# Kernel tuning notes

Hardware: AMD Instinct MI355X
Metric: run time of the kernel (lower is better)

## Reference

```python
import jax, jax.numpy as jnp
import numpy as np

H = 32          # num attention heads
KVH = 8         # num key/value heads
D = 128         # head dim
THETA = 10000.0


def _rope_tables(kv_len):
    inv_freq = 1.0 / (THETA ** (jnp.arange(0, D, 2, dtype=jnp.float32) / D))  # [D/2]
    t = jnp.arange(kv_len, dtype=jnp.float32)
    freqs = jnp.outer(t, inv_freq)                  # [kv_len, D/2]
    emb = jnp.concatenate([freqs, freqs], axis=-1)  # [kv_len, D]
    return jnp.cos(emb), jnp.sin(emb)


def _rotate_half(x):
    x1, x2 = jnp.split(x, 2, axis=-1)
    return jnp.concatenate([-x2, x1], axis=-1)


def setup_inputs() -> dict:
    key = jax.random.key(0)
    ks = jax.random.split(key, 7)
    B, QL, KVL, HID = 4, 128, 4096, 4096
    hidden_states = jax.random.normal(ks[0], (B, QL, HID), jnp.float32)
    key_states = jax.random.normal(ks[1], (B, KVH, KVL, D), jnp.float32)
    value_states = jax.random.normal(ks[2], (B, KVH, KVL, D), jnp.float32)
    Wq = jax.random.normal(ks[3], (HID, H * D), jnp.float32) * (HID ** -0.5)
    Wo = jax.random.normal(ks[4], (H * D, HID), jnp.float32) * ((H * D) ** -0.5)
    position_ids = jnp.sort(jax.random.randint(ks[5], (B, KVL), 0, KVL), axis=-1).astype(jnp.int64)
    attention_mask = jax.random.randint(ks[6], (B, 1, QL, KVL), 0, 2) == 1
    return {"hidden_states": hidden_states, "key_states": key_states,
            "value_states": value_states, "Wq": Wq, "Wo": Wo,
            "position_ids": position_ids, "attention_mask": attention_mask}


def reference(hidden_states, key_states, value_states, Wq, Wo, position_ids, attention_mask):
    B, QL, HID = hidden_states.shape
    KVL = position_ids.shape[-1]

    # q projection -> [B, H, QL, D]
    q = (hidden_states @ Wq).reshape(B, QL, H, D).transpose(0, 2, 1, 3)

    # RoPE: apply rotation for the single max position per batch to all q positions
    cos, sin = _rope_tables(KVL)                               # [KVL, D]
    pos = jnp.take_along_axis(position_ids,
                              jnp.argmax(position_ids.astype(jnp.int32), axis=1)[:, None],
                              axis=1)                          # [B, 1]
    cos_b = cos[pos][:, None]                                  # [B, 1, 1, D]
    sin_b = sin[pos][:, None]
    q = q * cos_b + _rotate_half(q) * sin_b

    # GQA repeat kv heads -> [B, H, KVL, D]
    groups = H // KVH
    k = jnp.repeat(key_states, groups, axis=1)
    v = jnp.repeat(value_states, groups, axis=1)

    scores = jnp.einsum('bhqd,bhkd->bhqk', q, k) / jnp.sqrt(jnp.float32(D))
    scores = jnp.where(attention_mask, jnp.float32(-10000.0), scores)
    attn = jax.nn.softmax(scores.astype(jnp.float32), axis=-1).astype(q.dtype)

    out = jnp.einsum('bhqk,bhkd->bhqd', attn, v)               # [B, H, QL, D]
    out = out.transpose(0, 2, 1, 3).reshape(B, QL, H * D)
    return out @ Wo
```

## Files before the change

### kernel.cpp

```cpp
#include <hip/hip_runtime.h>
#include <math.h>

typedef __attribute__((ext_vector_type(8))) short bf16x8;
typedef __attribute__((ext_vector_type(4))) float f32x4;
typedef __attribute__((ext_vector_type(4))) short s16x4;
typedef __attribute__((ext_vector_type(4))) int i32x4;

__device__ inline unsigned short f2bf(float x){
  unsigned u = __builtin_bit_cast(unsigned, x);
  u = (u + 0x7FFFu + ((u >> 16) & 1u)) >> 16;
  return (unsigned short)u;
}
__device__ inline float bf2f(unsigned short v){
  return __builtin_bit_cast(float, (unsigned)v << 16);
}
__device__ inline unsigned pk2bf(float lo, float hi){
  return (unsigned)f2bf(lo) | ((unsigned)f2bf(hi) << 16);
}

__device__ inline void gl16(const void* g, void* l){
  __builtin_amdgcn_global_load_lds(
      (const __attribute__((address_space(1))) unsigned int*)g,
      (__attribute__((address_space(3))) unsigned int*)l, 16, 0, 0);
}

#define KVLEN 4096
#define QLEN  128
#define NH    32
#define NKVH  8
#define HD    128
#define HIDD  4096
#define NSPLIT 4
#define KVCHUNK (KVLEN / NSPLIT)

#define WSWZ(n) ((((unsigned)(n) & 7u) ^ (((unsigned)(n) >> 3) & 7u)) << 4)
#define VSWZ(byte) ((byte) ^ ((((byte) >> 11) & 7u) << 4))

__global__ void prep_kernel(const int* __restrict__ pos32,
                            float* __restrict__ costab,
                            float* __restrict__ sintab){
  int tid = threadIdx.x;
  int b = tid >> 6, j = tid & 63;
  bool pos64 = (pos32[2*4095 + 1] == 0);
  long long mpos;
  if (pos64) mpos = ((const long long*)pos32)[(size_t)b*KVLEN + KVLEN - 1];
  else       mpos = (long long)pos32[(size_t)b*KVLEN + KVLEN - 1];
  double inv = pow(10000.0, -((double)j) / 64.0);
  double ang = (double)mpos * inv;
  costab[b*64 + j] = (float)cos(ang);
  sintab[b*64 + j] = (float)sin(ang);
}

__global__ __launch_bounds__(256) void prepall_kernel(
    const float* __restrict__ Kg, const float* __restrict__ Vg,
    const float* __restrict__ Wq, const float* __restrict__ Wo,
    const float* __restrict__ hidden, const void* __restrict__ mask,
    const float* __restrict__ costab, const float* __restrict__ sintab,
    unsigned short* __restrict__ Kswz, unsigned short* __restrict__ V2,
    unsigned short* __restrict__ WqImg, unsigned short* __restrict__ WoImg,
    unsigned short* __restrict__ A1img,
    unsigned long long* __restrict__ bits){
  __shared__ alignas(16) char tl[16384];
  int bid = blockIdx.x, tid = threadIdx.x;

  if (bid < 2048){
    const unsigned int* m32 = (const unsigned int*)mask;
    unsigned long long det = __ballot((m32[tid & 63] & 0xFFFFFF00u) != 0);
    bool m8 = (det != 0);
#pragma unroll
    for (int it = 0; it < 4; ++it){
      int idx = bid * 1024 + it * 256 + tid;
      bool v = m8 ? (((const unsigned char*)mask)[idx] != 0)
                  : (((const int*)mask)[idx] != 0);
      unsigned long long bal = __ballot(v);
      if ((tid & 63) == 0) bits[idx >> 6] = bal;
    }

  } else if (bid < 4096){
    int t = bid - 2048;
    int b = t >> 9;
    const float* kin = Kg + (size_t)t * 8192;
    const float* vin = Vg + (size_t)t * 8192;
    unsigned short* kout = Kswz + (size_t)t * 8192;
    unsigned short* vout = V2   + (size_t)t * 8192;
#pragma unroll
    for (int i = 0; i < 4; ++i){
      int c = tid + 256*i;
      int r = c >> 4, d0 = (c & 15) * 8;
      int dp = d0 ^ 64;
      bool low = d0 < 64;
      f32x4 x0 = *(const f32x4*)(kin + r*128 + d0);
      f32x4 x1 = *(const f32x4*)(kin + r*128 + d0 + 4);
      f32x4 y0 = *(const f32x4*)(kin + r*128 + dp);
      f32x4 y1 = *(const f32x4*)(kin + r*128 + dp + 4);
      int j0 = d0 & 63;
      bf16x8 s;
#pragma unroll
      for (int tt = 0; tt < 8; ++tt){
        float cc = costab[b*64 + j0 + tt];
        float ss = sintab[b*64 + j0 + tt];
        float x = (tt < 4) ? x0[tt] : x1[tt-4];
        float y = (tt < 4) ? y0[tt] : y1[tt-4];
        float v = low ? (x*cc + y*ss) : (x*cc - y*ss);
        s[tt] = (short)f2bf(v);
      }
      unsigned o = ((unsigned)(r*256 + d0*2)) ^ (((unsigned)r & 7u) << 4);
      *(bf16x8*)(tl + o) = s;
    }
    __syncthreads();
#pragma unroll
    for (int i = 0; i < 4; ++i)
      *(bf16x8*)((char*)kout + tid*16 + i*4096) = *(const bf16x8*)(tl + tid*16 + i*4096);
    __syncthreads();
#pragma unroll
    for (int i = 0; i < 4; ++i){
      int c = tid + 256*i;
      int r = c >> 4, d0 = (c & 15) * 8;
      f32x4 x0 = *(const f32x4*)(vin + r*128 + d0);
      f32x4 x1 = *(const f32x4*)(vin + r*128 + d0 + 4);
      int ks2 = r >> 5, lk4 = (r >> 3) & 3, e = r & 7;
#pragma unroll
      for (int tt = 0; tt < 8; ++tt){
        int d = d0 + tt;
        float v = (tt < 4) ? x0[tt] : x1[tt-4];
        unsigned cc = (unsigned)((((d >> 4)*2 + ks2)*4 + lk4)*16 + (d & 15));
        unsigned byte = cc*16u + (unsigned)e*2u;
        *(unsigned short*)(tl + VSWZ(byte)) = f2bf(v);
      }
    }
    __syncthreads();
#pragma unroll
    for (int i = 0; i < 4; ++i)
      *(bf16x8*)((char*)vout + tid*16 + i*4096) = *(const bf16x8*)(tl + tid*16 + i*4096);

  } else {
    int t = bid - 4096;
    if (t < 8192){
      const float* W = (t < 4096) ? Wq : Wo;
      unsigned short* img = (t < 4096) ? WqImg : WoImg;
      int tt = t & 4095;
      int kt = tt >> 6, bn = tt & 63;
      char* outB = (char*)img + (size_t)(bn*64 + kt) * 8192;
#pragma unroll
      for (int i = 0; i < 2; ++i){
        int c = tid + 256*i;
        int k = c >> 3, n0 = (c & 7) * 8;
        const float* src = W + (size_t)(kt*64 + k) * HIDD + bn*64 + n0;
        f32x4 x0 = *(const f32x4*)src;
        f32x4 x1 = *(const f32x4*)(src + 4);
#pragma unroll
        for (int e = 0; e < 8; ++e){
          int n = n0 + e;
          float v = (e < 4) ? x0[e] : x1[e-4];
          unsigned off = ((unsigned)(n*128 + k*2)) ^ WSWZ(n);
          *(unsigned short*)(tl + off) = f2bf(v);
        }
      }
      __syncthreads();
#pragma unroll
      for (int i = 0; i < 2; ++i)
        *(bf16x8*)(outB + tid*16 + i*4096) = *(const bf16x8*)(tl + tid*16 + i*4096);
    } else {
      int ta = t - 8192;
      int bm = ta >> 6, kt = ta & 63;
      char* outA = (char*)A1img + (size_t)ta * 8192;
#pragma unroll
      for (int i = 0; i < 2; ++i){
        int c = tid + 256*i;
        int m = c >> 3, kc = c & 7;
        const float* src = hidden + (size_t)(bm*64 + m) * HIDD + kt*64 + kc*8;
        f32x4 x0 = *(const f32x4*)src;
        f32x4 x1 = *(const f32x4*)(src + 4);
        bf16x8 s;
#pragma unroll
        for (int e = 0; e < 4; ++e){ s[e] = (short)f2bf(x0[e]); s[e+4] = (short)f2bf(x1[e]); }
        unsigned off = ((unsigned)(m*128 + kc*16)) ^ (((unsigned)m & 7u) << 4);
        *(bf16x8*)(tl + off) = s;
      }
      __syncthreads();
#pragma unroll
      for (int i = 0; i < 2; ++i)
        *(bf16x8*)(outA + tid*16 + i*4096) = *(const bf16x8*)(tl + tid*16 + i*4096);
    }
  }
}

template<int EPI>
__global__ __launch_bounds__(256, 2) void gemm_kernel(const unsigned short* __restrict__ Aimg,
                                                      const unsigned short* __restrict__ Bimg,
                                                      void* __restrict__ C_){
  __shared__ alignas(16) char smem[65536];
  int bid = blockIdx.x;
  int bn = (bid & 7) | ((bid >> 6) << 3);
  int bm = (bid >> 3) & 7;
  int tid = threadIdx.x, lane = tid & 63, w = tid >> 6;
  int wm = w >> 1, wn = w & 1;
  int l16 = lane & 15, lk4 = lane >> 4;
  const char* At = (const char*)Aimg + (size_t)(bm*64) * 8192;
  const char* Bt = (const char*)Bimg + (size_t)(bn*64) * 8192;
  f32x4 acc[2][2] = {};

#define GSTAGE(KT2, BUF) do { \
    const char* ga_ = At + (size_t)(KT2)*16384 + w*4096 + lane*16; \
    const char* gb_ = Bt + (size_t)(KT2)*16384 + w*4096 + lane*16; \
    char* la_ = smem + (BUF)*32768 + w*4096; \
    char* lb_ = smem + (BUF)*32768 + 16384 + w*4096; \
    _Pragma("unroll") for (int i_ = 0; i_ < 4; ++i_) gl16(ga_ + i_*1024, la_ + i_*1024); \
    _Pragma("unroll") for (int i_ = 0; i_ < 4; ++i_) gl16(gb_ + i_*1024, lb_ + i_*1024); \
  } while(0)

  GSTAGE(0, 0);

  for (int kt = 0; kt < 32; ++kt){
    asm volatile("s_waitcnt vmcnt(0)" ::: "memory");
    asm volatile("s_waitcnt lgkmcnt(0)" ::: "memory");
    __builtin_amdgcn_s_barrier();
    __builtin_amdgcn_sched_barrier(0);
    if (kt + 1 < 32) GSTAGE(kt + 1, (kt + 1) & 1);
    const char* Ab = smem + (kt & 1)*32768;
    const char* Bb = Ab + 16384;
    bf16x8 af[2][4], bfr[2][4];
#pragma unroll
    for (int i = 0; i < 2; ++i)
#pragma unroll
      for (int ks = 0; ks < 4; ++ks){
        unsigned m = (unsigned)(wm*32 + i*16 + l16);
        unsigned off = (unsigned)(ks >> 1)*8192u +
                       ((m*128u + (unsigned)((ks & 1)*64 + lk4*16)) ^ ((m & 7u) << 4));
        af[i][ks] = *(const bf16x8*)(Ab + off);
      }
#pragma unroll
    for (int j = 0; j < 2; ++j)
#pragma unroll
      for (int ks = 0; ks < 4; ++ks){
        unsigned n = (unsigned)(wn*32 + j*16 + l16);
        unsigned off = (unsigned)(ks >> 1)*8192u +
                       ((n*128u + (unsigned)((ks & 1)*64 + lk4*16)) ^ WSWZ(n));
        bfr[j][ks] = *(const bf16x8*)(Bb + off);
      }
#pragma unroll
    for (int i = 0; i < 2; ++i)
#pragma unroll
      for (int j = 0; j < 2; ++j)
#pragma unroll
        for (int ks = 0; ks < 4; ++ks)
          acc[i][j] = __builtin_amdgcn_mfma_f32_16x16x32_bf16(af[i][ks], bfr[j][ks], acc[i][j], 0, 0, 0);
  }
#undef GSTAGE

  if (EPI == 0){
    float* C = (float*)C_;
#pragma unroll
    for (int i = 0; i < 2; ++i)
#pragma unroll
      for (int j = 0; j < 2; ++j)
#pragma unroll
        for (int r = 0; r < 4; ++r){
          int row = bm*64 + wm*32 + i*16 + lk4*4 + r;
          int col = bn*64 + wn*32 + j*16 + l16;
          C[(size_t)row * HIDD + col] = acc[i][j][r];
        }
  } else {
    unsigned short* Q = (unsigned short*)C_;
    const float scale = 0.08838834764831845f * 1.4426950408889634f;
#pragma unroll
    for (int i = 0; i < 2; ++i)
#pragma unroll
      for (int j = 0; j < 2; ++j)
#pragma unroll
        for (int r = 0; r < 4; ++r){
          int row = bm*64 + wm*32 + i*16 + lk4*4 + r;
          int col = bn*64 + wn*32 + j*16 + l16;
          int b = row >> 7, ql = row & 127;
          int h = col >> 7, d = col & 127;
          Q[(((size_t)(b*NH + h)) * QLEN + ql) * HD + d] = f2bf(acc[i][j][r] * scale);
        }
  }
}

__global__ __launch_bounds__(256, 2) void attn_kernel(const unsigned short* __restrict__ Q,
                                                      const unsigned short* __restrict__ Kswz,
                                                      const unsigned short* __restrict__ V2,
                                                      const unsigned long long* __restrict__ bits,
                                                      unsigned short* __restrict__ Opart,
                                                      float* __restrict__ Mpart,
                                                      float* __restrict__ Lpart){
  __shared__ alignas(16) unsigned short Kbuf[2][8192];
  __shared__ alignas(16) unsigned short Vbuf[2][8192];
  int bid = blockIdx.x;
  int j = (bid >> 3) & 3;
  int g = (bid & 7) | ((bid >> 5) << 3);
  int s   = g & 3;
  int kvh = (g >> 2) & 7;
  int b   = g >> 5;
  int h   = kvh * 4 + j;

  int tid = threadIdx.x, lane = tid & 63, w = tid >> 6;
  int l16 = lane & 15, lk4 = lane >> 4;
  int lk4x4 = lk4 * 4;

  bf16x8 qf[2][4];
#pragma unroll
  for (int qg = 0; qg < 2; ++qg){
    const unsigned short* qp = Q + (((size_t)(b*NH + h) * QLEN) + w*32 + qg*16 + l16) * HD;
#pragma unroll
    for (int ks = 0; ks < 4; ++ks)
      qf[qg][ks] = *(const bf16x8*)(qp + ks*32 + lk4*8);
  }
  bf16x8 vone;
#pragma unroll
  for (int t = 0; t < 8; ++t) vone[t] = (short)0x3F80;

  f32x4 acc_o[2][8] = {};
  f32x4 acc_l[2] = {};
  float mrun[2] = {-1e30f, -1e30f};

  size_t kvhbase = (size_t)(b*NKVH + kvh) * (KVLEN/64);
  const unsigned short* Ktiles = Kswz + kvhbase * 8192;
  const unsigned short* Vtiles = V2   + kvhbase * 8192;
  size_t qrow0 = (size_t)(b*QLEN + w*32 + l16);

  const int t0 = s * (KVCHUNK/64), t1 = t0 + KVCHUNK/64;
  int srcb0 = (l16 + ((lk4 & 1) << 5)) << 2;
  int srcb1 = srcb0 + 64;

#define STAGE(T, BUF) do { \
    const char* gk_ = (const char*)(Ktiles + (size_t)(T)*8192) + w*4096 + lane*16; \
    const char* gv_ = (const char*)(Vtiles + (size_t)(T)*8192) + w*4096 + lane*16; \
    char* lk_ = (char*)(&Kbuf[BUF][0]) + w*4096; \
    char* lv_ = (char*)(&Vbuf[BUF][0]) + w*4096; \
    _Pragma("unroll") for (int i_ = 0; i_ < 4; ++i_) gl16(gk_ + i_*1024, lk_ + i_*1024); \
    _Pragma("unroll") for (int i_ = 0; i_ < 4; ++i_) gl16(gv_ + i_*1024, lv_ + i_*1024); \
  } while(0)

  STAGE(t0, 0);
  int cur = 0;
  for (int t = t0; t < t1; ++t){
    asm volatile("s_waitcnt vmcnt(0)" ::: "memory");
    asm volatile("s_waitcnt lgkmcnt(0)" ::: "memory");
    __builtin_amdgcn_s_barrier();
    __builtin_amdgcn_sched_barrier(0);
    if (t + 1 < t1) STAGE(t + 1, cur ^ 1);

    unsigned long long wrd[2];
    wrd[0] = bits[qrow0*64 + (size_t)t];
    wrd[1] = bits[(qrow0 + 16)*64 + (size_t)t];

    const char* Kc = (const char*)&Kbuf[cur][0];
    const char* Vc = (const char*)&Vbuf[cur][0];

    f32x4 sacc[2][4] = {};
#pragma unroll
    for (int nf = 0; nf < 4; ++nf){
      int krow = nf*16 + l16;
#pragma unroll
      for (int ks = 0; ks < 4; ++ks){
        unsigned byteoff = ((unsigned)krow*256u + (unsigned)(ks*32 + lk4*8)*2u) ^ (((unsigned)krow & 7u) << 4);
        bf16x8 kf = *(const bf16x8*)(Kc + byteoff);
        sacc[0][nf] = __builtin_amdgcn_mfma_f32_16x16x32_bf16(kf, qf[0][ks], sacc[0][nf], 0, 0, 0);
        sacc[1][nf] = __builtin_amdgcn_mfma_f32_16x16x32_bf16(kf, qf[1][ks], sacc[1][nf], 0, 0, 0);
      }
    }

    unsigned P32[2][8];
#pragma unroll
    for (int qg = 0; qg < 2; ++qg){
      float pp[4][4];
      float pm = -1e30f;
#pragma unroll
      for (int nf = 0; nf < 4; ++nf)
#pragma unroll
        for (int r = 0; r < 4; ++r){
          bool mk = (wrd[qg] >> (nf*16 + lk4x4 + r)) & 1ull;
          float sv = mk ? -20000.f : sacc[qg][nf][r];
          pp[nf][r] = sv;
          pm = fmaxf(pm, sv);
        }
      pm = fmaxf(pm, __shfl_xor(pm, 16, 64));
      pm = fmaxf(pm, __shfl_xor(pm, 32, 64));
      if (__any(pm > mrun[qg])){
        float mnew = fmaxf(mrun[qg], pm);
        float corr = exp2f(mrun[qg] - mnew);
        mrun[qg] = mnew;
#pragma unroll
        for (int nf8 = 0; nf8 < 8; ++nf8)
#pragma unroll
          for (int r = 0; r < 4; ++r) acc_o[qg][nf8][r] *= corr;
#pragma unroll
        for (int r = 0; r < 4; ++r) acc_l[qg][r] *= corr;
      }
#pragma unroll
      for (int nf = 0; nf < 4; ++nf){
        float e0 = exp2f(pp[nf][0] - mrun[qg]);
        float e1 = exp2f(pp[nf][1] - mrun[qg]);
        float e2 = exp2f(pp[nf][2] - mrun[qg]);
        float e3 = exp2f(pp[nf][3] - mrun[qg]);
        P32[qg][nf*2]     = pk2bf(e0, e1);
        P32[qg][nf*2 + 1] = pk2bf(e2, e3);
      }
    }

    bf16x8 pf[2][2];
    bool hi = lk4 >= 2;
#pragma unroll
    for (int qg = 0; qg < 2; ++qg)
#pragma unroll
      for (int ks2 = 0; ks2 < 2; ++ks2){
        int a0 = __builtin_amdgcn_ds_bpermute(srcb0, (int)P32[qg][ks2*4 + 0]);
        int b0 = __builtin_amdgcn_ds_bpermute(srcb0, (int)P32[qg][ks2*4 + 2]);
        int a1 = __builtin_amdgcn_ds_bpermute(srcb0, (int)P32[qg][ks2*4 + 1]);
        int b1 = __builtin_amdgcn_ds_bpermute(srcb0, (int)P32[qg][ks2*4 + 3]);
        int a2 = __builtin_amdgcn_ds_bpermute(srcb1, (int)P32[qg][ks2*4 + 0]);
        int b2 = __builtin_amdgcn_ds_bpermute(srcb1, (int)P32[qg][ks2*4 + 2]);
        int a3 = __builtin_amdgcn_ds_bpermute(srcb1, (int)P32[qg][ks2*4 + 1]);
        int b3 = __builtin_amdgcn_ds_bpermute(srcb1, (int)P32[qg][ks2*4 + 3]);
        i32x4 wv = { hi ? b0 : a0, hi ? b1 : a1, hi ? b2 : a2, hi ? b3 : a3 };
        pf[qg][ks2] = __builtin_bit_cast(bf16x8, wv);
      }

#pragma unroll
    for (int nf8 = 0; nf8 < 8; ++nf8)
#pragma unroll
      for (int ks2 = 0; ks2 < 2; ++ks2){
        unsigned base = (unsigned)(nf8*2 + ks2)*1024u + (unsigned)lane*16u;
        unsigned byteoff = VSWZ(base);
        bf16x8 vf = *(const bf16x8*)(Vc + byteoff);
        acc_o[0][nf8] = __builtin_amdgcn_mfma_f32_16x16x32_bf16(vf, pf[0][ks2], acc_o[0][nf8], 0, 0, 0);
        acc_o[1][nf8] = __builtin_amdgcn_mfma_f32_16x16x32_bf16(vf, pf[1][ks2], acc_o[1][nf8], 0, 0, 0);
      }
#pragma unroll
    for (int qg = 0; qg < 2; ++qg)
#pragma unroll
      for (int ks2 = 0; ks2 < 2; ++ks2)
        acc_l[qg] = __builtin_amdgcn_mfma_f32_16x16x32_bf16(vone, pf[qg][ks2], acc_l[qg], 0, 0, 0);

    cur ^= 1;
  }
#undef STAGE

  size_t rowbase = ((size_t)(s*4 + b) * NH + h) * QLEN + w*32 + l16;
#pragma unroll
  for (int qg = 0; qg < 2; ++qg){
    size_t row = rowbase + qg*16;
#pragma unroll
    for (int nf8 = 0; nf8 < 8; ++nf8){
      s16x4 o;
#pragma unroll
      for (int r = 0; r < 4; ++r) o[r] = (short)f2bf(acc_o[qg][nf8][r]);
      *(s16x4*)&Opart[row * HD + nf8*16 + lk4x4] = o;
    }
    if (lk4 == 0){
      Mpart[row] = mrun[qg];
      Lpart[row] = acc_l[qg][0];
    }
  }
}

__global__ __launch_bounds__(256) void combine_kernel(const unsigned short* __restrict__ Opart,
                                                      const float* __restrict__ Mpart,
                                                      const float* __restrict__ Lpart,
                                                      unsigned short* __restrict__ A2img){
  int idx = blockIdx.x * 256 + threadIdx.x;
  int d4 = idx & 31;
  int row = idx >> 5;
  const int RS = 4 * NH * QLEN;
  float m[NSPLIT];
  float M = -1e30f;
#pragma unroll
  for (int s = 0; s < NSPLIT; ++s){
    m[s] = Mpart[(size_t)s*RS + row];
    M = fmaxf(M, m[s]);
  }
  float L = 0.f;
  f32x4 num = {};
#pragma unroll
  for (int s = 0; s < NSPLIT; ++s){
    float wsc = exp2f(m[s] - M);
    L += wsc * Lpart[(size_t)s*RS + row];
    s16x4 o = *(const s16x4*)&Opart[((size_t)s*RS + row) * HD + d4*4];
#pragma unroll
    for (int t = 0; t < 4; ++t) num[t] += wsc * bf2f((unsigned short)o[t]);
  }
  int ql = row & 127, h = (row >> 7) & 31, b = row >> 12;
  int bm = b*2 + (ql >> 6), mm = ql & 63;
  int kt = h*2 + (d4 >> 4), kl = (d4*4) & 63;
  s16x4 res;
#pragma unroll
  for (int t = 0; t < 4; ++t) res[t] = (short)f2bf(num[t] / L);
  char* tile = (char*)A2img + (size_t)(bm*64 + kt) * 8192;
  unsigned off = ((unsigned)(mm*128 + kl*2)) ^ (((unsigned)mm & 7u) << 4);
  *(s16x4*)(tile + off) = res;
}

extern "C" void kernel_launch(void* const* d_in, const int* in_sizes, int n_in,
                              void* d_out, int out_size, void* d_ws, size_t ws_size,
                              hipStream_t stream){
  (void)in_sizes; (void)n_in; (void)out_size; (void)ws_size;
  const float* hidden = (const float*)d_in[0];
  const float* kst    = (const float*)d_in[1];
  const float* vst    = (const float*)d_in[2];
  const float* wq     = (const float*)d_in[3];
  const float* wo     = (const float*)d_in[4];
  const void*  pos    = d_in[5];
  const void*  mask   = d_in[6];
  float* out = (float*)d_out;

  char* ws = (char*)d_ws;
  unsigned short* Kswz  = (unsigned short*)ws;
  unsigned short* V2    = (unsigned short*)(ws + (32u << 20));
  unsigned short* WoImg = (unsigned short*)(ws + (64u << 20));
  unsigned short* WqImg = (unsigned short*)(ws + (96u << 20));
  unsigned short* Opart = (unsigned short*)(ws + (96u << 20));
  unsigned short* A1img = (unsigned short*)(ws + (128u << 20));
  unsigned short* qbf   = (unsigned short*)(ws + (132u << 20));
  unsigned short* A2img = (unsigned short*)(ws + (136u << 20));
  float* Mpart = (float*)(ws + (140u << 20));
  float* Lpart = (float*)(ws + (140u << 20) + (256u << 10));
  unsigned long long* bits = (unsigned long long*)(ws + (140u << 20) + (512u << 10));
  float* costab = (float*)(ws + (141u << 20));
  float* sintab = costab + 256;

  prep_kernel<<<1, 256, 0, stream>>>((const int*)pos, costab, sintab);
  prepall_kernel<<<12800, 256, 0, stream>>>(kst, vst, wq, wo, hidden, mask,
                                            costab, sintab,
                                            Kswz, V2, WqImg, WoImg, A1img, bits);
  gemm_kernel<1><<<512, 256, 0, stream>>>(A1img, WqImg, qbf);
  attn_kernel<<<512, 256, 0, stream>>>(qbf, Kswz, V2, bits, Opart, Mpart, Lpart);
  combine_kernel<<<2048, 256, 0, stream>>>(Opart, Mpart, Lpart, A2img);
  gemm_kernel<0><<<512, 256, 0, stream>>>(A2img, WoImg, out);
}
```

Baseline: 208.1 us.

## Fuse fp32 weight-to-bf16 conversion into GEMM B-tile loading

Drops the separate prep pass that turned Wq and Wo into swizzled bf16 images. Each GEMM now reads fp32 weight rows directly into registers, converts them to bf16 and writes the swizzled B tile into shared memory, double-buffered against the MFMA loop. This removes a full write and re-read of 64 MB of bf16 weight images and shrinks the prep grid. In exchange the GEMM reads twice as many weight bytes as fp32, spends registers on staging, and waits on the B loads synchronously each iteration instead of using async LDS loads.

```diff
diff --git a/kernel.cpp b/kernel.cpp
--- a/kernel.cpp
+++ b/kernel.cpp
@@ -53,11 +53,9 @@
 
 __global__ __launch_bounds__(256) void prepall_kernel(
     const float* __restrict__ Kg, const float* __restrict__ Vg,
-    const float* __restrict__ Wq, const float* __restrict__ Wo,
     const float* __restrict__ hidden, const void* __restrict__ mask,
     const float* __restrict__ costab, const float* __restrict__ sintab,
     unsigned short* __restrict__ Kswz, unsigned short* __restrict__ V2,
-    unsigned short* __restrict__ WqImg, unsigned short* __restrict__ WoImg,
     unsigned short* __restrict__ A1img,
     unsigned long long* __restrict__ bits){
   __shared__ alignas(16) char tl[16384];
@@ -134,60 +132,32 @@
       *(bf16x8*)((char*)vout + tid*16 + i*4096) = *(const bf16x8*)(tl + tid*16 + i*4096);
 
   } else {
-    int t = bid - 4096;
-    if (t < 8192){
-      const float* W = (t < 4096) ? Wq : Wo;
-      unsigned short* img = (t < 4096) ? WqImg : WoImg;
-      int tt = t & 4095;
-      int kt = tt >> 6, bn = tt & 63;
-      char* outB = (char*)img + (size_t)(bn*64 + kt) * 8192;
-#pragma unroll
-      for (int i = 0; i < 2; ++i){
-        int c = tid + 256*i;
-        int k = c >> 3, n0 = (c & 7) * 8;
-        const float* src = W + (size_t)(kt*64 + k) * HIDD + bn*64 + n0;
-        f32x4 x0 = *(const f32x4*)src;
-        f32x4 x1 = *(const f32x4*)(src + 4);
-#pragma unroll
-        for (int e = 0; e < 8; ++e){
-          int n = n0 + e;
-          float v = (e < 4) ? x0[e] : x1[e-4];
-          unsigned off = ((unsigned)(n*128 + k*2)) ^ WSWZ(n);
-          *(unsigned short*)(tl + off) = f2bf(v);
-        }
-      }
-      __syncthreads();
-#pragma unroll
-      for (int i = 0; i < 2; ++i)
-        *(bf16x8*)(outB + tid*16 + i*4096) = *(const bf16x8*)(tl + tid*16 + i*4096);
-    } else {
-      int ta = t - 8192;
-      int bm = ta >> 6, kt = ta & 63;
-      char* outA = (char*)A1img + (size_t)ta * 8192;
-#pragma unroll
-      for (int i = 0; i < 2; ++i){
-        int c = tid + 256*i;
-        int m = c >> 3, kc = c & 7;
-        const float* src = hidden + (size_t)(bm*64 + m) * HIDD + kt*64 + kc*8;
-        f32x4 x0 = *(const f32x4*)src;
-        f32x4 x1 = *(const f32x4*)(src + 4);
-        bf16x8 s;
-#pragma unroll
-        for (int e = 0; e < 4; ++e){ s[e] = (short)f2bf(x0[e]); s[e+4] = (short)f2bf(x1[e]); }
-        unsigned off = ((unsigned)(m*128 + kc*16)) ^ (((unsigned)m & 7u) << 4);
-        *(bf16x8*)(tl + off) = s;
-      }
-      __syncthreads();
-#pragma unroll
-      for (int i = 0; i < 2; ++i)
-        *(bf16x8*)(outA + tid*16 + i*4096) = *(const bf16x8*)(tl + tid*16 + i*4096);
-    }
+    int ta = bid - 4096;
+    int bm = ta >> 6, kt = ta & 63;
+    char* outA = (char*)A1img + (size_t)ta * 8192;
+#pragma unroll
+    for (int i = 0; i < 2; ++i){
+      int c = tid + 256*i;
+      int m = c >> 3, kc = c & 7;
+      const float* src = hidden + (size_t)(bm*64 + m) * HIDD + kt*64 + kc*8;
+      f32x4 x0 = *(const f32x4*)src;
+      f32x4 x1 = *(const f32x4*)(src + 4);
+      bf16x8 s;
+#pragma unroll
+      for (int e = 0; e < 4; ++e){ s[e] = (short)f2bf(x0[e]); s[e+4] = (short)f2bf(x1[e]); }
+      unsigned off = ((unsigned)(m*128 + kc*16)) ^ (((unsigned)m & 7u) << 4);
+      *(bf16x8*)(tl + off) = s;
+    }
+    __syncthreads();
+#pragma unroll
+    for (int i = 0; i < 2; ++i)
+      *(bf16x8*)(outA + tid*16 + i*4096) = *(const bf16x8*)(tl + tid*16 + i*4096);
   }
 }
 
 template<int EPI>
 __global__ __launch_bounds__(256, 2) void gemm_kernel(const unsigned short* __restrict__ Aimg,
-                                                      const unsigned short* __restrict__ Bimg,
+                                                      const float* __restrict__ W,
                                                       void* __restrict__ C_){
   __shared__ alignas(16) char smem[65536];
   int bid = blockIdx.x;
@@ -197,68 +167,86 @@
   int wm = w >> 1, wn = w & 1;
   int l16 = lane & 15, lk4 = lane >> 4;
   const char* At = (const char*)Aimg + (size_t)(bm*64) * 8192;
-  const char* Bt = (const char*)Bimg + (size_t)(bn*64) * 8192;
+  int n4 = (tid & 15) * 4;
+  int kb = (tid >> 4) * 8;
+  const float* Wt = W + (size_t)kb * HIDD + (size_t)bn * 64 + n4;
+  f32x4 breg[8];
   f32x4 acc[2][2] = {};
 
-#define GSTAGE(KT2, BUF) do { \
+#define LOADB(KT2) do { \
+    _Pragma("unroll") for (int e_ = 0; e_ < 8; ++e_) \
+      breg[e_] = *(const f32x4*)(Wt + ((size_t)(KT2)*128 + e_) * HIDD); \
+  } while(0)
+#define WRITEB(BUF) do { \
+    _Pragma("unroll") for (int c_ = 0; c_ < 4; ++c_){ \
+      bf16x8 pk_; \
+      _Pragma("unroll") for (int e_ = 0; e_ < 8; ++e_) pk_[e_] = (short)f2bf(breg[e_][c_]); \
+      unsigned nn_ = (unsigned)(n4 + c_); \
+      unsigned off_ = (nn_*256u + (unsigned)kb*2u) ^ WSWZ(nn_); \
+      *(bf16x8*)(smem + (BUF)*32768 + 16384 + off_) = pk_; \
+    } } while(0)
+#define LOADA(KT2, BUF) do { \
     const char* ga_ = At + (size_t)(KT2)*16384 + w*4096 + lane*16; \
-    const char* gb_ = Bt + (size_t)(KT2)*16384 + w*4096 + lane*16; \
     char* la_ = smem + (BUF)*32768 + w*4096; \
-    char* lb_ = smem + (BUF)*32768 + 16384 + w*4096; \
     _Pragma("unroll") for (int i_ = 0; i_ < 4; ++i_) gl16(ga_ + i_*1024, la_ + i_*1024); \
-    _Pragma("unroll") for (int i_ = 0; i_ < 4; ++i_) gl16(gb_ + i_*1024, lb_ + i_*1024); \
   } while(0)
 
-  GSTAGE(0, 0);
-
+  LOADB(0);
+  LOADA(0, 0);
+  asm volatile("s_waitcnt vmcnt(0)" ::: "memory");
+  WRITEB(0);
+
+  int cur = 0;
   for (int kt = 0; kt < 32; ++kt){
-    asm volatile("s_waitcnt vmcnt(0)" ::: "memory");
+    if (kt + 1 < 32){ LOADB(kt + 1); LOADA(kt + 1, cur ^ 1); }
     asm volatile("s_waitcnt lgkmcnt(0)" ::: "memory");
     __builtin_amdgcn_s_barrier();
     __builtin_amdgcn_sched_barrier(0);
-    if (kt + 1 < 32) GSTAGE(kt + 1, (kt + 1) & 1);
-    const char* Ab = smem + (kt & 1)*32768;
+    const char* Ab = smem + cur*32768;
     const char* Bb = Ab + 16384;
-    bf16x8 af[2][4], bfr[2][4];
-#pragma unroll
-    for (int i = 0; i < 2; ++i)
-#pragma unroll
-      for (int ks = 0; ks < 4; ++ks){
+#pragma unroll
+    for (int ks = 0; ks < 4; ++ks){
+      bf16x8 af[2], bfr[2];
+#pragma unroll
+      for (int i = 0; i < 2; ++i){
         unsigned m = (unsigned)(wm*32 + i*16 + l16);
         unsigned off = (unsigned)(ks >> 1)*8192u +
                        ((m*128u + (unsigned)((ks & 1)*64 + lk4*16)) ^ ((m & 7u) << 4));
-        af[i][ks] = *(const bf16x8*)(Ab + off);
-      }
-#pragma unroll
-    for (int j = 0; j < 2; ++j)
-#pragma unroll
-      for (int ks = 0; ks < 4; ++ks){
-        unsigned n = (unsigned)(wn*32 + j*16 + l16);
-        unsigned off = (unsigned)(ks >> 1)*8192u +
-                       ((n*128u + (unsigned)((ks & 1)*64 + lk4*16)) ^ WSWZ(n));
-        bfr[j][ks] = *(const bf16x8*)(Bb + off);
-      }
-#pragma unroll
-    for (int i = 0; i < 2; ++i)
-#pragma unroll
-      for (int j = 0; j < 2; ++j)
-#pragma unroll
-        for (int ks = 0; ks < 4; ++ks)
-          acc[i][j] = __builtin_amdgcn_mfma_f32_16x16x32_bf16(af[i][ks], bfr[j][ks], acc[i][j], 0, 0, 0);
-  }
-#undef GSTAGE
+        af[i] = *(const bf16x8*)(Ab + off);
+      }
+#pragma unroll
+      for (int jj = 0; jj < 2; ++jj){
+        unsigned n = (unsigned)(wn*32 + jj*16 + l16);
+        unsigned off = (n*256u + (unsigned)(ks*64 + lk4*16)) ^ WSWZ(n);
+        bfr[jj] = *(const bf16x8*)(Bb + off);
+      }
+#pragma unroll
+      for (int i = 0; i < 2; ++i)
+#pragma unroll
+        for (int jj = 0; jj < 2; ++jj)
+          acc[i][jj] = __builtin_amdgcn_mfma_f32_16x16x32_bf16(af[i], bfr[jj], acc[i][jj], 0, 0, 0);
+    }
+    if (kt + 1 < 32){
+      asm volatile("s_waitcnt vmcnt(0)" ::: "memory");
+      WRITEB(cur ^ 1);
+    }
+    cur ^= 1;
+  }
+#undef LOADB
+#undef WRITEB
+#undef LOADA
 
   if (EPI == 0){
     float* C = (float*)C_;
 #pragma unroll
     for (int i = 0; i < 2; ++i)
 #pragma unroll
-      for (int j = 0; j < 2; ++j)
+      for (int jj = 0; jj < 2; ++jj)
 #pragma unroll
         for (int r = 0; r < 4; ++r){
           int row = bm*64 + wm*32 + i*16 + lk4*4 + r;
-          int col = bn*64 + wn*32 + j*16 + l16;
-          C[(size_t)row * HIDD + col] = acc[i][j][r];
+          int col = bn*64 + wn*32 + jj*16 + l16;
+          C[(size_t)row * HIDD + col] = acc[i][jj][r];
         }
   } else {
     unsigned short* Q = (unsigned short*)C_;
@@ -266,14 +254,14 @@
 #pragma unroll
     for (int i = 0; i < 2; ++i)
 #pragma unroll
-      for (int j = 0; j < 2; ++j)
+      for (int jj = 0; jj < 2; ++jj)
 #pragma unroll
         for (int r = 0; r < 4; ++r){
           int row = bm*64 + wm*32 + i*16 + lk4*4 + r;
-          int col = bn*64 + wn*32 + j*16 + l16;
+          int col = bn*64 + wn*32 + jj*16 + l16;
           int b = row >> 7, ql = row & 127;
           int h = col >> 7, d = col & 127;
-          Q[(((size_t)(b*NH + h)) * QLEN + ql) * HD + d] = f2bf(acc[i][j][r] * scale);
+          Q[(((size_t)(b*NH + h)) * QLEN + ql) * HD + d] = f2bf(acc[i][jj][r] * scale);
         }
   }
 }
@@ -508,24 +496,22 @@
   char* ws = (char*)d_ws;
   unsigned short* Kswz  = (unsigned short*)ws;
   unsigned short* V2    = (unsigned short*)(ws + (32u << 20));
-  unsigned short* WoImg = (unsigned short*)(ws + (64u << 20));
-  unsigned short* WqImg = (unsigned short*)(ws + (96u << 20));
-  unsigned short* Opart = (unsigned short*)(ws + (96u << 20));
-  unsigned short* A1img = (unsigned short*)(ws + (128u << 20));
-  unsigned short* qbf   = (unsigned short*)(ws + (132u << 20));
-  unsigned short* A2img = (unsigned short*)(ws + (136u << 20));
-  float* Mpart = (float*)(ws + (140u << 20));
-  float* Lpart = (float*)(ws + (140u << 20) + (256u << 10));
-  unsigned long long* bits = (unsigned long long*)(ws + (140u << 20) + (512u << 10));
-  float* costab = (float*)(ws + (141u << 20));
+  unsigned short* Opart = (unsigned short*)(ws + (64u << 20));
+  unsigned short* A1img = (unsigned short*)(ws + (80u << 20));
+  unsigned short* qbf   = (unsigned short*)(ws + (84u << 20));
+  unsigned short* A2img = (unsigned short*)(ws + (88u << 20));
+  float* Mpart = (float*)(ws + (92u << 20));
+  float* Lpart = (float*)(ws + (92u << 20) + (256u << 10));
+  unsigned long long* bits = (unsigned long long*)(ws + (92u << 20) + (512u << 10));
+  float* costab = (float*)(ws + (93u << 20));
   float* sintab = costab + 256;
 
   prep_kernel<<<1, 256, 0, stream>>>((const int*)pos, costab, sintab);
-  prepall_kernel<<<12800, 256, 0, stream>>>(kst, vst, wq, wo, hidden, mask,
-                                            costab, sintab,
-                                            Kswz, V2, WqImg, WoImg, A1img, bits);
-  gemm_kernel<1><<<512, 256, 0, stream>>>(A1img, WqImg, qbf);
+  prepall_kernel<<<4608, 256, 0, stream>>>(kst, vst, hidden, mask,
+                                           costab, sintab,
+                                           Kswz, V2, A1img, bits);
+  gemm_kernel<1><<<512, 256, 0, stream>>>(A1img, wq, qbf);
   attn_kernel<<<512, 256, 0, stream>>>(qbf, Kswz, V2, bits, Opart, Mpart, Lpart);
   combine_kernel<<<2048, 256, 0, stream>>>(Opart, Mpart, Lpart, A2img);
-  gemm_kernel<0><<<512, 256, 0, stream>>>(A2img, WoImg, out);
-}
+  gemm_kernel<0><<<512, 256, 0, stream>>>(A2img, wo, out);
+}
```

After: 231.4 us. 1.11x slower.
